# Kernel optimization log

Measured on AMD Instinct MI355X. Metric: run time of the kernel, lower is better.

Reference implementation:

```python
import jax, jax.numpy as jnp
import numpy as np

NUM_GROUPS = 32
EPS = 1e-6


def group_norm(x, gamma, beta):
    # x: [b, c, d, h, w]
    b, c, d, h, w = x.shape
    xg = x.reshape(b, NUM_GROUPS, c // NUM_GROUPS, d, h, w)
    mean = jnp.mean(xg, axis=(2, 3, 4, 5), keepdims=True)
    var = jnp.var(xg, axis=(2, 3, 4, 5), keepdims=True)
    xn = ((xg - mean) * jax.lax.rsqrt(var + EPS)).reshape(b, c, d, h, w)
    return xn * gamma[None, :, None, None, None] + beta[None, :, None, None, None]


def conv1x1(x, w, bias):
    # 1x1x1 conv == channel-mixing matmul. x: [b,c,d,h,w], w: [co,ci]
    y = jnp.einsum('oc,bcdhw->bodhw', w, x)
    return y + bias[None, :, None, None, None]


def setup_inputs() -> dict:
    key = jax.random.key(0)
    ks = jax.random.split(key, 12)
    b, c, d, h, w = 2, 512, 16, 16, 16
    scale = 1.0 / np.sqrt(c)
    inp = {
        'x': jax.random.normal(ks[0], (b, c, d, h, w), dtype=jnp.float32),
        'gamma': jnp.ones((c,), dtype=jnp.float32),
        'beta': jnp.zeros((c,), dtype=jnp.float32),
        'wq': jax.random.normal(ks[1], (c, c), dtype=jnp.float32) * scale,
        'bq': jnp.zeros((c,), dtype=jnp.float32),
        'wk': jax.random.normal(ks[2], (c, c), dtype=jnp.float32) * scale,
        'bk': jnp.zeros((c,), dtype=jnp.float32),
        'wv': jax.random.normal(ks[3], (c, c), dtype=jnp.float32) * scale,
        'bv': jnp.zeros((c,), dtype=jnp.float32),
        'wo': jax.random.normal(ks[4], (c, c), dtype=jnp.float32) * scale,
        'bo': jnp.zeros((c,), dtype=jnp.float32),
    }
    return inp


def reference(x, gamma, beta, wq, bq, wk, bk, wv, bv, wo, bo):
    b, c, d, h, w = x.shape
    n = d * h * w
    h_ = group_norm(x, gamma, beta)
    q = conv1x1(h_, wq, bq).reshape(b, c, n)  # [b,c,n]
    k = conv1x1(h_, wk, bk).reshape(b, c, n)
    v = conv1x1(h_, wv, bv).reshape(b, c, n)
    scale = jnp.float32(c) ** -0.5
    # attn[b, i, j] = sum_c q[b,c,i] * k[b,c,j]
    attn = jnp.einsum('bci,bcj->bij', q, k) * scale
    attn = jax.nn.softmax(attn, axis=2)
    # out[b, c, i] = sum_j attn[b,i,j] * v[b,c,j]
    o = jnp.einsum('bij,bcj->bci', attn, v).reshape(b, c, d, h, w)
    return x + conv1x1(o, wo, bo)
```

## Files before the change

kernel.cpp:

```cpp
#include <hip/hip_runtime.h>
#include <hip/hip_bf16.h>

typedef __bf16 bf16x8 __attribute__((ext_vector_type(8)));
typedef _Float16 f16x8 __attribute__((ext_vector_type(8)));
typedef unsigned short u16x8 __attribute__((ext_vector_type(8)));
typedef float f32x4 __attribute__((ext_vector_type(4)));
using bf16 = __hip_bfloat16;

constexpr int Cdim = 512;
constexpr int Nsp  = 4096;
constexpr int NB   = 2;
constexpr float SCALE = 0.04419417382415922f;
constexpr int EPITCH = 132;

#define GL2LDS(gaddr, laddr)                                                              \
    __builtin_amdgcn_global_load_lds((const __attribute__((address_space(1))) void*)(gaddr), \
                                     (__attribute__((address_space(3))) void*)(laddr), 16, 0, 0)

#define STG1(dst, src, ld) { int _o = tid * 16, _r = _o >> 7, _c = ((_o >> 4) ^ _r) & 7;      \
    GL2LDS((const unsigned short*)(src) + (size_t)_r * (ld) + _c * 8,                          \
           (unsigned short*)(dst) + (_o >> 1)); }

__global__ __launch_bounds__(256) void k_cvt_all(const float* __restrict__ wq, const float* __restrict__ wk,
                                                 const float* __restrict__ wv, const float* __restrict__ wo,
                                                 bf16* __restrict__ wqkb, bf16* __restrict__ wvb,
                                                 bf16* __restrict__ wob, float* __restrict__ lsum) {
    if (blockIdx.x >= 256) {
        #pragma unroll
        for (int j = 0; j < 8; ++j)
            ((float4*)lsum)[8 * threadIdx.x + j] = float4{0.f, 0.f, 0.f, 0.f};
        return;
    }
    int i = blockIdx.x * 256 + threadIdx.x;
    float4 q = ((const float4*)wq)[i];
    float4 k = ((const float4*)wk)[i];
    float4 v = ((const float4*)wv)[i];
    float4 o = ((const float4*)wo)[i];
    bf16* dq = wqkb + (size_t)i * 4;
    dq[0] = __float2bfloat16(q.x); dq[1] = __float2bfloat16(q.y);
    dq[2] = __float2bfloat16(q.z); dq[3] = __float2bfloat16(q.w);
    bf16* dk = wqkb + 262144 + (size_t)i * 4;
    dk[0] = __float2bfloat16(k.x); dk[1] = __float2bfloat16(k.y);
    dk[2] = __float2bfloat16(k.z); dk[3] = __float2bfloat16(k.w);
    bf16* dv = wvb + (size_t)i * 4;
    dv[0] = __float2bfloat16(v.x); dv[1] = __float2bfloat16(v.y);
    dv[2] = __float2bfloat16(v.z); dv[3] = __float2bfloat16(v.w);
    bf16* dw = wob + (size_t)i * 4;
    dw[0] = __float2bfloat16(o.x); dw[1] = __float2bfloat16(o.y);
    dw[2] = __float2bfloat16(o.z); dw[3] = __float2bfloat16(o.w);
}

__global__ __launch_bounds__(256) void k_gn_stats(const float* __restrict__ x, float* __restrict__ stats) {
    int bg = blockIdx.x;
    const float4* p = (const float4*)(x + (size_t)bg * (16 * 4096));
    float s = 0.f, s2 = 0.f;
    for (int i = threadIdx.x; i < 16384; i += 256) {
        float4 v = p[i];
        s  += v.x + v.y + v.z + v.w;
        s2 += v.x * v.x + v.y * v.y + v.z * v.z + v.w * v.w;
    }
    #pragma unroll
    for (int off = 32; off; off >>= 1) { s += __shfl_xor(s, off); s2 += __shfl_xor(s2, off); }
    __shared__ float rs[4], rs2[4];
    int w = threadIdx.x >> 6;
    if ((threadIdx.x & 63) == 0) { rs[w] = s; rs2[w] = s2; }
    __syncthreads();
    if (threadIdx.x == 0) {
        float S = rs[0] + rs[1] + rs[2] + rs[3];
        float S2 = rs2[0] + rs2[1] + rs2[2] + rs2[3];
        float mean = S * (1.f / 65536.f);
        float var  = S2 * (1.f / 65536.f) - mean * mean;
        stats[bg * 2]     = mean;
        stats[bg * 2 + 1] = rsqrtf(var + 1e-6f);
    }
}

__global__ __launch_bounds__(256) void k_gn_apply(const float* __restrict__ x, const float* __restrict__ stats,
                                                  const float* __restrict__ gamma, const float* __restrict__ beta,
                                                  bf16* __restrict__ ht) {
    int b = blockIdx.y;
    int n0 = blockIdx.x * 64;
    int tid = threadIdx.x;
    __shared__ float tile[64][65];
    int nn_l = tid & 63, cc0 = tid >> 6;
    int cc_w = tid & 63, nn0 = tid >> 6;
    for (int c0 = 0; c0 < Cdim; c0 += 64) {
        #pragma unroll
        for (int p = 0; p < 16; ++p) {
            int cc = p * 4 + cc0;
            tile[cc][nn_l] = x[(size_t)(b * Cdim + c0 + cc) * Nsp + n0 + nn_l];
        }
        __syncthreads();
        int c = c0 + cc_w, g = c >> 4;
        float mean = stats[(b * 32 + g) * 2];
        float rstd = stats[(b * 32 + g) * 2 + 1];
        float ga = gamma[c], be = beta[c];
        #pragma unroll
        for (int p = 0; p < 16; ++p) {
            int nn = p * 4 + nn0;
            float v = tile[cc_w][nn];
            ht[(size_t)(b * Nsp + n0 + nn) * Cdim + c] = __float2bfloat16((v - mean) * rstd * ga + be);
        }
        __syncthreads();
    }
}

template <int DT>
__device__ __forceinline__ f32x4 mma16(u16x8 a, u16x8 b, f32x4 c) {
    if constexpr (DT == 0)
        return __builtin_amdgcn_mfma_f32_16x16x32_bf16(__builtin_bit_cast(bf16x8, a),
                                                       __builtin_bit_cast(bf16x8, b), c, 0, 0, 0);
    else
        return __builtin_amdgcn_mfma_f32_16x16x32_f16(__builtin_bit_cast(f16x8, a),
                                                      __builtin_bit_cast(f16x8, b), c, 0, 0, 0);
}

template <int BM, int DT, int OUTT, int BIAS, int RESID, int SPLITK, int EXPSUM>
__global__ __launch_bounds__(256) void k_gemm_nt(
    const void* __restrict__ Av, long long As, int lda,
    const void* __restrict__ Bv, long long Bs, int ldb,
    const float* __restrict__ bias, const float* __restrict__ bias2,
    const float* __restrict__ resid, long long Rs,
    float* __restrict__ lsum,
    void* __restrict__ outv, long long Os,
    int N, int K) {
    constexpr int MT = BM / 32;
    constexpr int SME_STAGE = (BM + 128) * 64;
    constexpr int SME_EPI   = BM * EPITCH;
    constexpr int SME = SME_STAGE > SME_EPI ? SME_STAGE : SME_EPI;
    const int bm = blockIdx.x, bn = blockIdx.y, zz = blockIdx.z;
    const int bt  = (SPLITK > 1) ? (zz % NB) : zz;
    const int ksl = (SPLITK > 1) ? (zz / NB) : 0;
    const int Kc = K / SPLITK;
    const int kbeg = ksl * Kc;
    const unsigned short* Ab = (const unsigned short*)Av + (size_t)bt * As;
    const unsigned short* Bb = (const unsigned short*)Bv + (size_t)bt * Bs;
    const int tid = threadIdx.x, lane = tid & 63, w = tid >> 6;
    const int quad = lane >> 4, l16 = lane & 15;
    const int wm = w >> 1, wn = w & 1;
    __shared__ __align__(16) unsigned short smem[SME];
    unsigned short (*Asub)[64] = (unsigned short(*)[64])smem;
    unsigned short (*Bsub)[64] = (unsigned short(*)[64])(smem + BM * 64);
    f32x4 zero4 = {0.f, 0.f, 0.f, 0.f};
    f32x4 acc[MT][4];
    #pragma unroll
    for (int i = 0; i < MT; ++i)
        #pragma unroll
        for (int j = 0; j < 4; ++j) acc[i][j] = zero4;
    const int row0 = bm * BM, col0 = bn * 128;
    const size_t ldab = (size_t)lda * 2, ldbb = (size_t)ldb * 2;
    const int lsw = (l16 & 7) * 8;
    for (int k0 = kbeg; k0 < kbeg + Kc; k0 += 64) {
        const char* Abase = (const char*)Ab + (size_t)k0 * 2;
        const char* Bbase = (const char*)Bb + (size_t)k0 * 2;
        #pragma unroll
        for (int p = 0; p < BM / 32; ++p) {
            int o = p * 4096 + tid * 16;
            int r = o >> 7;
            int cs = ((o >> 4) ^ r) & 7;
            GL2LDS(Abase + (size_t)(row0 + r) * ldab + cs * 16, (char*)smem + o);
        }
        #pragma unroll
        for (int p = 0; p < 4; ++p) {
            int o = p * 4096 + tid * 16;
            int r = o >> 7;
            int cs = ((o >> 4) ^ r) & 7;
            GL2LDS(Bbase + (size_t)(col0 + r) * ldbb + cs * 16, (char*)smem + BM * 128 + o);
        }
        __syncthreads();
        #pragma unroll
        for (int ks = 0; ks < 2; ++ks) {
            u16x8 af[MT], bfr[4];
            #pragma unroll
            for (int t = 0; t < MT; ++t)
                af[t] = *(const u16x8*)&Asub[wm * (BM / 2) + t * 16 + l16][(ks * 32 + quad * 8) ^ lsw];
            #pragma unroll
            for (int t = 0; t < 4; ++t)
                bfr[t] = *(const u16x8*)&Bsub[wn * 64 + t * 16 + l16][(ks * 32 + quad * 8) ^ lsw];
            #pragma unroll
            for (int tm = 0; tm < MT; ++tm)
                #pragma unroll
                for (int tn = 0; tn < 4; ++tn) acc[tm][tn] = mma16<DT>(af[tm], bfr[tn], acc[tm][tn]);
        }
        __syncthreads();
    }

    if constexpr (OUTT == 2) {
        #pragma unroll
        for (int tm = 0; tm < MT; ++tm)
            #pragma unroll
            for (int tn = 0; tn < 4; ++tn)
                #pragma unroll
                for (int r = 0; r < 4; ++r) {
                    int row = row0 + wm * (BM / 2) + tm * 16 + quad * 4 + r;
                    int col = col0 + wn * 64 + tn * 16 + l16;
                    float v = acc[tm][tn][r];
                    if constexpr (BIAS == 1) v += bias[row];
                    else if constexpr (BIAS == 2) v += bias[col];
                    if constexpr (RESID) v += resid[(size_t)bt * Rs + (size_t)row * N + col];
                    ((float*)outv)[(size_t)zz * Os + (size_t)row * N + col] = v;
                }
    } else {
        #pragma unroll
        for (int tn = 0; tn < 4; ++tn) {
            int colL = wn * 64 + tn * 16 + l16;
            float bc = 0.f;
            if constexpr (BIAS == 2) bc = bias[col0 + colL];
            else if constexpr (BIAS == 3) {
                int col = col0 + colL;
                bc = (col < 512) ? bias[col] : bias2[col - 512];
            }
            #pragma unroll
            for (int tm = 0; tm < MT; ++tm)
                #pragma unroll
                for (int r = 0; r < 4; ++r) {
                    int rowL = wm * (BM / 2) + tm * 16 + quad * 4 + r;
                    float v = acc[tm][tn][r];
                    if constexpr (BIAS == 1) v += bias[row0 + rowL];
                    else if constexpr (BIAS == 2) v += bc;
                    else if constexpr (BIAS == 3) {
                        int col = col0 + colL;
                        v = (col < 512) ? (v + bc) * SCALE : v + bc;
                    }
                    if constexpr (EXPSUM) v = __expf(v);
                    unsigned short hv;
                    if constexpr (OUTT == 1) { _Float16 h = (_Float16)v; hv = __builtin_bit_cast(unsigned short, h); }
                    else { bf16 h = __float2bfloat16(v); hv = __builtin_bit_cast(unsigned short, h); }
                    smem[rowL * EPITCH + colL] = hv;
                }
        }
        __syncthreads();
        const int cch = (tid & 15) * 8;
        const int rg  = (tid >> 4) * (BM / 16);
        #pragma unroll
        for (int i = 0; i < BM / 16; ++i) {
            int rowL = rg + i;
            u16x8 hv = *(const u16x8*)&smem[rowL * EPITCH + cch];
            *(u16x8*)((unsigned short*)outv + (size_t)zz * Os + (size_t)(row0 + rowL) * N + col0 + cch) = hv;
            if constexpr (EXPSUM) {
                float ps = 0.f;
                #pragma unroll
                for (int e = 0; e < 8; ++e) {
                    bf16 h = __builtin_bit_cast(bf16, hv[e]);
                    ps += __bfloat162float(h);
                }
                #pragma unroll
                for (int m = 1; m < 16; m <<= 1) ps += __shfl_xor(ps, m);
                if ((lane & 15) == 0) atomicAdd(lsum + (size_t)bt * Nsp + row0 + rowL, ps);
            }
        }
    }
}

__global__ __launch_bounds__(512, 2) void k_attn(const bf16* __restrict__ QKt_, const bf16* __restrict__ Vm_,
                                                 float* __restrict__ lsum, bf16* __restrict__ Opart_) {
    constexpr int NT = 32;
    const int bx = blockIdx.x, js = blockIdx.y, bt = blockIdx.z;
    const int i0 = bx * 64;
    const int jbase = js * 2048;
    const unsigned short* Qb = (const unsigned short*)QKt_ + (size_t)bt * ((size_t)Nsp * 1024);
    const unsigned short* Vb = (const unsigned short*)Vm_ + (size_t)bt * ((size_t)Nsp * Cdim);
    const int tid = threadIdx.x, lane = tid & 63, w = tid >> 6;
    const int quad = lane >> 4, l16 = lane & 15;
    const int wm = w >> 2, wn = w & 3;
    const int lsw = (l16 & 7) * 8;
    __shared__ __align__(16) unsigned short smem[69632];
    unsigned short* Q_l = smem;
    unsigned short* H0  = smem + 32768;
    unsigned short* H1  = smem + 49152;
    unsigned short* P_l = smem + 65536;

#define FR(sub, row, kc) (*(const u16x8*)&(sub)[(row) * 64 + ((kc) ^ lsw)])
#define PH_TOP() \
    __builtin_amdgcn_s_barrier(); \
    asm volatile("s_waitcnt lgkmcnt(0)" ::: "memory"); \
    __builtin_amdgcn_sched_barrier(0); \
    __builtin_amdgcn_s_setprio(1);

    f32x4 zero4 = {0.f, 0.f, 0.f, 0.f};
    f32x4 acc[2][8];
    #pragma unroll
    for (int m = 0; m < 2; ++m)
        #pragma unroll
        for (int n = 0; n < 8; ++n) acc[m][n] = zero4;
    float rsum[2][4] = {{0.f, 0.f, 0.f, 0.f}, {0.f, 0.f, 0.f, 0.f}};
    u16x8 pa[2][2];
    u16x8 fb[8];

    #pragma unroll
    for (int s = 0; s < 8; ++s) STG1(Q_l + s * 4096, Qb + (size_t)i0 * 1024 + s * 64, 1024);
    #pragma unroll
    for (int s = 0; s < 4; ++s) STG1(H0 + s * 4096, Qb + (size_t)jbase * 1024 + 512 + s * 64, 1024);
    asm volatile("s_waitcnt vmcnt(0)" ::: "memory");
    __builtin_amdgcn_s_barrier();
    __builtin_amdgcn_sched_barrier(0);

    for (int t = 0; t < NT; ++t) {
        const int j0 = jbase + t * 64;
        f32x4 aS[2] = {zero4, zero4};
        #pragma unroll
        for (int ks = 0; ks < 8; ++ks)
            fb[ks] = FR(H0 + (ks >> 1) * 4096, wn * 16 + l16, (ks & 1) * 32 + quad * 8);
        #pragma unroll
        for (int s = 0; s < 4; ++s)
            STG1(H1 + s * 4096, Qb + (size_t)j0 * 1024 + 512 + 256 + s * 64, 1024);
        PH_TOP();
        #pragma unroll
        for (int ks = 0; ks < 8; ++ks)
            #pragma unroll
            for (int m = 0; m < 2; ++m) {
                u16x8 aq = FR(Q_l + (ks >> 1) * 4096, wm * 32 + m * 16 + l16, (ks & 1) * 32 + quad * 8);
                aS[m] = mma16<0>(aq, fb[ks], aS[m]);
            }
        __builtin_amdgcn_s_setprio(0);
        asm volatile("s_waitcnt vmcnt(0)" ::: "memory");
        __builtin_amdgcn_s_barrier();
        #pragma unroll
        for (int ks = 0; ks < 8; ++ks)
            fb[ks] = FR(H1 + (ks >> 1) * 4096, wn * 16 + l16, (ks & 1) * 32 + quad * 8);
        #pragma unroll
        for (int s = 0; s < 4; ++s)
            STG1(H0 + s * 4096, Vb + (size_t)(s * 64) * 4096 + j0, 4096);
        PH_TOP();
        #pragma unroll
        for (int ks = 0; ks < 8; ++ks)
            #pragma unroll
            for (int m = 0; m < 2; ++m) {
                u16x8 aq = FR(Q_l + (4 + (ks >> 1)) * 4096, wm * 32 + m * 16 + l16, (ks & 1) * 32 + quad * 8);
                aS[m] = mma16<0>(aq, fb[ks], aS[m]);
            }
        __builtin_amdgcn_s_setprio(0);
        __builtin_amdgcn_s_barrier();
        #pragma unroll
        for (int s = 0; s < 4; ++s)
            STG1(H1 + s * 4096, Vb + (size_t)(256 + s * 64) * 4096 + j0, 4096);
        #pragma unroll
        for (int m = 0; m < 2; ++m)
            #pragma unroll
            for (int r = 0; r < 4; ++r) {
                float p = __expf(aS[m][r]);
                rsum[m][r] += p;
                int il = wm * 32 + m * 16 + quad * 4 + r;
                bf16 h = __float2bfloat16(p);
                P_l[il * 64 + ((wn * 16 + l16) ^ ((il & 7) * 8))] = __builtin_bit_cast(unsigned short, h);
            }
        asm volatile("s_waitcnt lgkmcnt(0)" ::: "memory");
        asm volatile("s_waitcnt vmcnt(4)" ::: "memory");
        __builtin_amdgcn_s_barrier();
        __builtin_amdgcn_sched_barrier(0);
        #pragma unroll
        for (int nn = 0; nn < 4; ++nn)
            #pragma unroll
            for (int ks = 0; ks < 2; ++ks)
                fb[nn * 2 + ks] = FR(H0 + wn * 4096, nn * 16 + l16, ks * 32 + quad * 8);
        PH_TOP();
        #pragma unroll
        for (int m = 0; m < 2; ++m)
            #pragma unroll
            for (int ks = 0; ks < 2; ++ks)
                pa[m][ks] = *(const u16x8*)&P_l[(wm * 32 + m * 16 + l16) * 64 + ((ks * 32 + quad * 8) ^ lsw)];
        #pragma unroll
        for (int m = 0; m < 2; ++m)
            #pragma unroll
            for (int nn = 0; nn < 4; ++nn)
                #pragma unroll
                for (int ks = 0; ks < 2; ++ks)
                    acc[m][nn] = mma16<0>(pa[m][ks], fb[nn * 2 + ks], acc[m][nn]);
        __builtin_amdgcn_s_setprio(0);
        asm volatile("s_waitcnt vmcnt(0)" ::: "memory");
        __builtin_amdgcn_s_barrier();
        #pragma unroll
        for (int nn = 0; nn < 4; ++nn)
            #pragma unroll
            for (int ks = 0; ks < 2; ++ks)
                fb[nn * 2 + ks] = FR(H1 + wn * 4096, nn * 16 + l16, ks * 32 + quad * 8);
        if (t + 1 < NT) {
            #pragma unroll
            for (int s = 0; s < 4; ++s)
                STG1(H0 + s * 4096, Qb + (size_t)(j0 + 64) * 1024 + 512 + s * 64, 1024);
        }
        PH_TOP();
        #pragma unroll
        for (int m = 0; m < 2; ++m)
            #pragma unroll
            for (int nn = 0; nn < 4; ++nn)
                #pragma unroll
                for (int ks = 0; ks < 2; ++ks)
                    acc[m][4 + nn] = mma16<0>(pa[m][ks], fb[nn * 2 + ks], acc[m][4 + nn]);
        __builtin_amdgcn_s_setprio(0);
        asm volatile("s_waitcnt vmcnt(0)" ::: "memory");
        __builtin_amdgcn_s_barrier();
        __builtin_amdgcn_sched_barrier(0);
    }
#undef FR
#undef PH_TOP

    #pragma unroll
    for (int m = 0; m < 2; ++m)
        #pragma unroll
        for (int r = 0; r < 4; ++r) {
            float v = rsum[m][r];
            v += __shfl_xor(v, 1); v += __shfl_xor(v, 2); v += __shfl_xor(v, 4); v += __shfl_xor(v, 8);
            if (l16 == 0)
                atomicAdd(lsum + (size_t)bt * Nsp + i0 + wm * 32 + m * 16 + quad * 4 + r, v);
        }
    __syncthreads();
    #pragma unroll
    for (int m = 0; m < 2; ++m)
        #pragma unroll
        for (int h = 0; h < 2; ++h)
            #pragma unroll
            for (int nn = 0; nn < 4; ++nn) {
                int colL = h * 256 + wn * 64 + nn * 16 + l16;
                int rowB = wm * 32 + m * 16 + quad * 4;
                #pragma unroll
                for (int r = 0; r < 4; ++r) {
                    int rw = rowB + r;
                    bf16 hv = __float2bfloat16(acc[m][h * 4 + nn][r]);
                    smem[rw * 520 + (colL ^ ((rw & 7) * 8))] = __builtin_bit_cast(unsigned short, hv);
                }
            }
    __syncthreads();
    const int orow = tid >> 3, ocb = tid & 7;
    unsigned short* od = (unsigned short*)Opart_ + (size_t)js * ((size_t)NB * Nsp * Cdim) +
                         ((size_t)bt * Nsp + i0 + orow) * Cdim;
    #pragma unroll
    for (int it = 0; it < 8; ++it) {
        int cc = ocb + it * 8;
        u16x8 hv = *(const u16x8*)&smem[orow * 520 + ((cc * 8) ^ ((orow & 7) * 8))];
        *(u16x8*)(od + cc * 8) = hv;
    }
}

__global__ __launch_bounds__(256) void k_reduce2(const bf16* __restrict__ P, const float* __restrict__ lsum,
                                                 bf16* __restrict__ O) {
    constexpr size_t SL = (size_t)NB * Nsp * Cdim;
    size_t i = ((size_t)blockIdx.x * 256 + threadIdx.x) * 8;
    float linv = 1.f / lsum[i >> 9];
    union { bf16 h[8]; uint4 u; } a, b, r;
    a.u = *(const uint4*)(P + i);
    b.u = *(const uint4*)(P + SL + i);
    #pragma unroll
    for (int e = 0; e < 8; ++e) {
        float s = __bfloat162float(a.h[e]) + __bfloat162float(b.h[e]);
        r.h[e] = __float2bfloat16(s * linv);
    }
    *(uint4*)(O + i) = r.u;
}

extern "C" void kernel_launch(void* const* d_in, const int* in_sizes, int n_in,
                              void* d_out, int out_size, void* d_ws, size_t ws_size,
                              hipStream_t stream) {
    const float* x     = (const float*)d_in[0];
    const float* gamma = (const float*)d_in[1];
    const float* beta  = (const float*)d_in[2];
    const float* wq = (const float*)d_in[3];  const float* bq = (const float*)d_in[4];
    const float* wk = (const float*)d_in[5];  const float* bk = (const float*)d_in[6];
    const float* wv = (const float*)d_in[7];  const float* bv = (const float*)d_in[8];
    const float* wo = (const float*)d_in[9];  const float* bo = (const float*)d_in[10];
    float* out = (float*)d_out;

    char* ws = (char*)d_ws;
    float* stats = (float*)ws;
    size_t off = 1024;
    float* lsum = (float*)(ws + off); off += (size_t)NB * Nsp * 4 + 1024;
    bf16* wqkb = (bf16*)(ws + off); off += (size_t)1024 * 512 * 2;
    bf16* wvb  = (bf16*)(ws + off); off += (size_t)512 * 512 * 2;
    bf16* wob  = (bf16*)(ws + off); off += (size_t)512 * 512 * 2;
    bf16* Vm   = (bf16*)(ws + off); off += (size_t)NB * Nsp * Cdim * 2;
    bf16* Ot   = (bf16*)(ws + off); off += (size_t)NB * Nsp * Cdim * 2;
    bf16* Opart = (bf16*)(ws + off); off += (size_t)2 * NB * Nsp * Cdim * 2;
    bf16* ht   = (bf16*)(ws + off); off += (size_t)NB * Nsp * Cdim * 2;
    bf16* QKt  = (bf16*)(ws + off); off += (size_t)NB * Nsp * 1024 * 2;

    k_cvt_all<<<257, 256, 0, stream>>>(wq, wk, wv, wo, wqkb, wvb, wob, lsum);
    k_gn_stats<<<64, 256, 0, stream>>>(x, stats);
    k_gn_apply<<<dim3(64, 2), 256, 0, stream>>>(x, stats, gamma, beta, ht);

    const long long hs = (long long)Nsp * Cdim;
    const long long qs = (long long)Nsp * 1024;

    k_gemm_nt<128, 0, 0, 3, 0, 1, 0><<<dim3(32, 8, 2), 256, 0, stream>>>(
        ht, hs, 512, wqkb, 0, 512, bq, bk, nullptr, 0, nullptr, QKt, qs, 1024, 512);
    k_gemm_nt<128, 0, 0, 1, 0, 1, 0><<<dim3(4, 32, 2), 256, 0, stream>>>(
        wvb, 0, 512, ht, hs, 512, bv, nullptr, nullptr, 0, nullptr, Vm, hs, 4096, 512);
    k_attn<<<dim3(64, 2, 2), 512, 0, stream>>>(QKt, Vm, lsum, Opart);
    k_reduce2<<<2048, 256, 0, stream>>>(Opart, lsum, Ot);
    k_gemm_nt<128, 0, 2, 1, 1, 1, 0><<<dim3(4, 32, 2), 256, 0, stream>>>(
        wob, 0, 512, Ot, hs, 512, bo, nullptr, x, hs, nullptr, out, hs, 4096, 512);
}
```

Before: 253.1 us.

## Hold Q fragments in registers and deepen K/V prefetch across four LDS slots

The attention kernel now loads its Q tile from LDS into registers once (qa[2][16]), which frees the Q region of shared memory. That space is reused so K halves and V halves each get their own buffer, four slots in total. Global-to-LDS loads for the next K/V pieces are issued earlier and tracked with partial vmcnt waits instead of full drains, aiming to overlap memory traffic with MFMA work and remove stalls. The cost is many more VGPRs for the Q fragments, which may cut occupancy or cause spills at launch_bounds(512,2), and more fragile wait-count bookkeeping.

```diff
diff --git a/kernel.cpp b/kernel.cpp
--- a/kernel.cpp
+++ b/kernel.cpp
@@ -265,17 +265,20 @@
     const int wm = w >> 2, wn = w & 3;
     const int lsw = (l16 & 7) * 8;
     __shared__ __align__(16) unsigned short smem[69632];
-    unsigned short* Q_l = smem;
-    unsigned short* H0  = smem + 32768;
-    unsigned short* H1  = smem + 49152;
     unsigned short* P_l = smem + 65536;
 
-#define FR(sub, row, kc) (*(const u16x8*)&(sub)[(row) * 64 + ((kc) ^ lsw)])
-#define PH_TOP() \
-    __builtin_amdgcn_s_barrier(); \
-    asm volatile("s_waitcnt lgkmcnt(0)" ::: "memory"); \
-    __builtin_amdgcn_sched_barrier(0); \
-    __builtin_amdgcn_s_setprio(1);
+    auto stgK = [&](int jj, int dh, unsigned short* dst) {
+        #pragma unroll
+        for (int s = 0; s < 4; ++s)
+            STG1(dst + s * 4096, Qb + (size_t)jj * 1024 + 512 + dh * 256 + s * 64, 1024);
+    };
+    auto stgV = [&](int jj, int ch, unsigned short* dst) {
+        #pragma unroll
+        for (int s = 0; s < 4; ++s)
+            STG1(dst + s * 4096, Vb + (size_t)(ch * 256 + s * 64) * 4096 + jj, 4096);
+    };
+
+#define FRD(base, row, kc) (*(const u16x8*)&(base)[(row) * 64 + ((kc) ^ lsw)])
 
     f32x4 zero4 = {0.f, 0.f, 0.f, 0.f};
     f32x4 acc[2][8];
@@ -285,55 +288,74 @@
         for (int n = 0; n < 8; ++n) acc[m][n] = zero4;
     float rsum[2][4] = {{0.f, 0.f, 0.f, 0.f}, {0.f, 0.f, 0.f, 0.f}};
     u16x8 pa[2][2];
-    u16x8 fb[8];
-
-    #pragma unroll
-    for (int s = 0; s < 8; ++s) STG1(Q_l + s * 4096, Qb + (size_t)i0 * 1024 + s * 64, 1024);
-    #pragma unroll
-    for (int s = 0; s < 4; ++s) STG1(H0 + s * 4096, Qb + (size_t)jbase * 1024 + 512 + s * 64, 1024);
-    asm volatile("s_waitcnt vmcnt(0)" ::: "memory");
+
+    #pragma unroll
+    for (int s = 0; s < 8; ++s) STG1(smem + s * 4096, Qb + (size_t)i0 * 1024 + s * 64, 1024);
+    stgK(jbase, 0, smem + 2 * 16384);
+    stgK(jbase, 1, smem + 3 * 16384);
+    asm volatile("s_waitcnt vmcnt(8)" ::: "memory");
     __builtin_amdgcn_s_barrier();
     __builtin_amdgcn_sched_barrier(0);
+    u16x8 qa[2][16];
+    #pragma unroll
+    for (int m = 0; m < 2; ++m)
+        #pragma unroll
+        for (int ks = 0; ks < 16; ++ks)
+            qa[m][ks] = FRD(smem + (ks >> 1) * 4096, wm * 32 + m * 16 + l16, (ks & 1) * 32 + quad * 8);
+    asm volatile("s_waitcnt lgkmcnt(0)" ::: "memory");
+    __builtin_amdgcn_s_barrier();
+    __builtin_amdgcn_sched_barrier(0);
+    stgV(jbase, 0, smem);
+
+#define PH_WAIT(N) \
+    asm volatile("s_waitcnt vmcnt(" #N ")" ::: "memory"); \
+    __builtin_amdgcn_s_barrier(); \
+    __builtin_amdgcn_sched_barrier(0);
+#define S_CLUSTER(KSL, QOFF) { \
+    u16x8 kb[8]; \
+    _Pragma("unroll") \
+    for (int ks = 0; ks < 8; ++ks) \
+        kb[ks] = FRD((KSL) + (ks >> 1) * 4096, wn * 16 + l16, (ks & 1) * 32 + quad * 8); \
+    asm volatile("s_waitcnt lgkmcnt(0)" ::: "memory"); \
+    __builtin_amdgcn_sched_barrier(0); \
+    __builtin_amdgcn_s_setprio(1); \
+    _Pragma("unroll") \
+    for (int ks = 0; ks < 8; ++ks) \
+        _Pragma("unroll") \
+        for (int m = 0; m < 2; ++m) aS[m] = mma16<0>(qa[m][(QOFF) + ks], kb[ks], aS[m]); \
+    __builtin_amdgcn_s_setprio(0); \
+    __builtin_amdgcn_s_barrier(); }
+#define PV_CLUSTER(VSL, HOFF) { \
+    u16x8 fb[4][2]; \
+    _Pragma("unroll") \
+    for (int nn = 0; nn < 4; ++nn) \
+        _Pragma("unroll") \
+        for (int ks = 0; ks < 2; ++ks) \
+            fb[nn][ks] = FRD((VSL) + wn * 4096, nn * 16 + l16, ks * 32 + quad * 8); \
+    asm volatile("s_waitcnt lgkmcnt(0)" ::: "memory"); \
+    __builtin_amdgcn_sched_barrier(0); \
+    __builtin_amdgcn_s_setprio(1); \
+    _Pragma("unroll") \
+    for (int m = 0; m < 2; ++m) \
+        _Pragma("unroll") \
+        for (int nn = 0; nn < 4; ++nn) \
+            _Pragma("unroll") \
+            for (int ks = 0; ks < 2; ++ks) \
+                acc[m][(HOFF) + nn] = mma16<0>(pa[m][ks], fb[nn][ks], acc[m][(HOFF) + nn]); \
+    __builtin_amdgcn_s_setprio(0); \
+    __builtin_amdgcn_s_barrier(); }
 
     for (int t = 0; t < NT; ++t) {
         const int j0 = jbase + t * 64;
+        const int j1 = j0 + 64;
         f32x4 aS[2] = {zero4, zero4};
-        #pragma unroll
-        for (int ks = 0; ks < 8; ++ks)
-            fb[ks] = FR(H0 + (ks >> 1) * 4096, wn * 16 + l16, (ks & 1) * 32 + quad * 8);
-        #pragma unroll
-        for (int s = 0; s < 4; ++s)
-            STG1(H1 + s * 4096, Qb + (size_t)j0 * 1024 + 512 + 256 + s * 64, 1024);
-        PH_TOP();
-        #pragma unroll
-        for (int ks = 0; ks < 8; ++ks)
-            #pragma unroll
-            for (int m = 0; m < 2; ++m) {
-                u16x8 aq = FR(Q_l + (ks >> 1) * 4096, wm * 32 + m * 16 + l16, (ks & 1) * 32 + quad * 8);
-                aS[m] = mma16<0>(aq, fb[ks], aS[m]);
-            }
-        __builtin_amdgcn_s_setprio(0);
-        asm volatile("s_waitcnt vmcnt(0)" ::: "memory");
-        __builtin_amdgcn_s_barrier();
-        #pragma unroll
-        for (int ks = 0; ks < 8; ++ks)
-            fb[ks] = FR(H1 + (ks >> 1) * 4096, wn * 16 + l16, (ks & 1) * 32 + quad * 8);
-        #pragma unroll
-        for (int s = 0; s < 4; ++s)
-            STG1(H0 + s * 4096, Vb + (size_t)(s * 64) * 4096 + j0, 4096);
-        PH_TOP();
-        #pragma unroll
-        for (int ks = 0; ks < 8; ++ks)
-            #pragma unroll
-            for (int m = 0; m < 2; ++m) {
-                u16x8 aq = FR(Q_l + (4 + (ks >> 1)) * 4096, wm * 32 + m * 16 + l16, (ks & 1) * 32 + quad * 8);
-                aS[m] = mma16<0>(aq, fb[ks], aS[m]);
-            }
-        __builtin_amdgcn_s_setprio(0);
-        __builtin_amdgcn_s_barrier();
-        #pragma unroll
-        for (int s = 0; s < 4; ++s)
-            STG1(H1 + s * 4096, Vb + (size_t)(256 + s * 64) * 4096 + j0, 4096);
+        stgV(j0, 1, smem + 1 * 16384);
+        PH_WAIT(12)
+        S_CLUSTER(smem + 2 * 16384, 0)
+        if (t + 1 < NT) { stgK(j1, 0, smem + 2 * 16384); PH_WAIT(12) }
+        else            { PH_WAIT(8) }
+        S_CLUSTER(smem + 3 * 16384, 8)
+        if (t + 1 < NT) stgK(j1, 1, smem + 3 * 16384);
         #pragma unroll
         for (int m = 0; m < 2; ++m)
             #pragma unroll
@@ -345,55 +367,21 @@
                 P_l[il * 64 + ((wn * 16 + l16) ^ ((il & 7) * 8))] = __builtin_bit_cast(unsigned short, h);
             }
         asm volatile("s_waitcnt lgkmcnt(0)" ::: "memory");
-        asm volatile("s_waitcnt vmcnt(4)" ::: "memory");
-        __builtin_amdgcn_s_barrier();
-        __builtin_amdgcn_sched_barrier(0);
-        #pragma unroll
-        for (int nn = 0; nn < 4; ++nn)
-            #pragma unroll
-            for (int ks = 0; ks < 2; ++ks)
-                fb[nn * 2 + ks] = FR(H0 + wn * 4096, nn * 16 + l16, ks * 32 + quad * 8);
-        PH_TOP();
+        if (t + 1 < NT) { PH_WAIT(12) } else { PH_WAIT(4) }
         #pragma unroll
         for (int m = 0; m < 2; ++m)
             #pragma unroll
             for (int ks = 0; ks < 2; ++ks)
                 pa[m][ks] = *(const u16x8*)&P_l[(wm * 32 + m * 16 + l16) * 64 + ((ks * 32 + quad * 8) ^ lsw)];
-        #pragma unroll
-        for (int m = 0; m < 2; ++m)
-            #pragma unroll
-            for (int nn = 0; nn < 4; ++nn)
-                #pragma unroll
-                for (int ks = 0; ks < 2; ++ks)
-                    acc[m][nn] = mma16<0>(pa[m][ks], fb[nn * 2 + ks], acc[m][nn]);
-        __builtin_amdgcn_s_setprio(0);
-        asm volatile("s_waitcnt vmcnt(0)" ::: "memory");
-        __builtin_amdgcn_s_barrier();
-        #pragma unroll
-        for (int nn = 0; nn < 4; ++nn)
-            #pragma unroll
-            for (int ks = 0; ks < 2; ++ks)
-                fb[nn * 2 + ks] = FR(H1 + wn * 4096, nn * 16 + l16, ks * 32 + quad * 8);
-        if (t + 1 < NT) {
-            #pragma unroll
-            for (int s = 0; s < 4; ++s)
-                STG1(H0 + s * 4096, Qb + (size_t)(j0 + 64) * 1024 + 512 + s * 64, 1024);
-        }
-        PH_TOP();
-        #pragma unroll
-        for (int m = 0; m < 2; ++m)
-            #pragma unroll
-            for (int nn = 0; nn < 4; ++nn)
-                #pragma unroll
-                for (int ks = 0; ks < 2; ++ks)
-                    acc[m][4 + nn] = mma16<0>(pa[m][ks], fb[nn * 2 + ks], acc[m][4 + nn]);
-        __builtin_amdgcn_s_setprio(0);
-        asm volatile("s_waitcnt vmcnt(0)" ::: "memory");
-        __builtin_amdgcn_s_barrier();
-        __builtin_amdgcn_sched_barrier(0);
-    }
-#undef FR
-#undef PH_TOP
+        PV_CLUSTER(smem, 0)
+        if (t + 1 < NT) { stgV(j1, 0, smem); PH_WAIT(12) }
+        else            { PH_WAIT(0) }
+        PV_CLUSTER(smem + 1 * 16384, 4)
+    }
+#undef FRD
+#undef PH_WAIT
+#undef S_CLUSTER
+#undef PV_CLUSTER
 
     #pragma unroll
     for (int m = 0; m < 2; ++m)
```

Result: slower. 345.4 us (+36.5%).

## Triple-buffer K/V tiles with rotating LDS buffers and register-resident Q fragment

Applied to the files above, without the earlier changes.

Restructures the attention main loop into a three-buffer rotation (A/B/C) so each K or V half-tile load is issued two phases ahead, with partial vmcnt waits instead of full drains. The low half of Q is held in registers for the whole loop, freeing the LDS space that backs the third buffer, while the high half of Q stays in LDS. This aims to hide global-to-LDS latency and cut stalls at barriers. In exchange it raises register pressure from the extra Q fragments, which at launch bounds of 512 threads and 2 blocks could cause spills, and the vmcnt accounting is fragile.

```diff
diff --git a/kernel.cpp b/kernel.cpp
--- a/kernel.cpp
+++ b/kernel.cpp
@@ -265,17 +265,25 @@
     const int wm = w >> 2, wn = w & 3;
     const int lsw = (l16 & 7) * 8;
     __shared__ __align__(16) unsigned short smem[69632];
-    unsigned short* Q_l = smem;
-    unsigned short* H0  = smem + 32768;
-    unsigned short* H1  = smem + 49152;
+    unsigned short* Qhi = smem + 49152;
     unsigned short* P_l = smem + 65536;
 
-#define FR(sub, row, kc) (*(const u16x8*)&(sub)[(row) * 64 + ((kc) ^ lsw)])
-#define PH_TOP() \
+    auto stgK = [&](int jj, int dh, unsigned short* dst) {
+        #pragma unroll
+        for (int s = 0; s < 4; ++s)
+            STG1(dst + s * 4096, Qb + (size_t)jj * 1024 + 512 + dh * 256 + s * 64, 1024);
+    };
+    auto stgV = [&](int jj, int ch, unsigned short* dst) {
+        #pragma unroll
+        for (int s = 0; s < 4; ++s)
+            STG1(dst + s * 4096, Vb + (size_t)(ch * 256 + s * 64) * 4096 + jj, 4096);
+    };
+
+#define FRD(base, row, kc) (*(const u16x8*)&(base)[(row) * 64 + ((kc) ^ lsw)])
+#define WAIT_BAR(N) \
+    asm volatile("s_waitcnt vmcnt(" #N ")" ::: "memory"); \
     __builtin_amdgcn_s_barrier(); \
-    asm volatile("s_waitcnt lgkmcnt(0)" ::: "memory"); \
-    __builtin_amdgcn_sched_barrier(0); \
-    __builtin_amdgcn_s_setprio(1);
+    __builtin_amdgcn_sched_barrier(0);
 
     f32x4 zero4 = {0.f, 0.f, 0.f, 0.f};
     f32x4 acc[2][8];
@@ -285,55 +293,69 @@
         for (int n = 0; n < 8; ++n) acc[m][n] = zero4;
     float rsum[2][4] = {{0.f, 0.f, 0.f, 0.f}, {0.f, 0.f, 0.f, 0.f}};
     u16x8 pa[2][2];
-    u16x8 fb[8];
-
-    #pragma unroll
-    for (int s = 0; s < 8; ++s) STG1(Q_l + s * 4096, Qb + (size_t)i0 * 1024 + s * 64, 1024);
-    #pragma unroll
-    for (int s = 0; s < 4; ++s) STG1(H0 + s * 4096, Qb + (size_t)jbase * 1024 + 512 + s * 64, 1024);
-    asm volatile("s_waitcnt vmcnt(0)" ::: "memory");
+
+    unsigned short* A = smem;
+    unsigned short* B = smem + 16384;
+    unsigned short* C = smem + 32768;
+
+    #pragma unroll
+    for (int s = 0; s < 4; ++s) STG1(C + s * 4096, Qb + (size_t)i0 * 1024 + s * 64, 1024);
+    #pragma unroll
+    for (int s = 0; s < 4; ++s) STG1(Qhi + s * 4096, Qb + (size_t)i0 * 1024 + 256 + s * 64, 1024);
+    stgK(jbase, 0, A);
+    stgK(jbase, 1, B);
+    WAIT_BAR(8)
+    u16x8 qa[2][8];
+    #pragma unroll
+    for (int m = 0; m < 2; ++m)
+        #pragma unroll
+        for (int ks = 0; ks < 8; ++ks)
+            qa[m][ks] = FRD(C + (ks >> 1) * 4096, wm * 32 + m * 16 + l16, (ks & 1) * 32 + quad * 8);
+    asm volatile("s_waitcnt lgkmcnt(0)" ::: "memory");
     __builtin_amdgcn_s_barrier();
     __builtin_amdgcn_sched_barrier(0);
 
     for (int t = 0; t < NT; ++t) {
         const int j0 = jbase + t * 64;
+        const int j1 = j0 + 64;
         f32x4 aS[2] = {zero4, zero4};
-        #pragma unroll
-        for (int ks = 0; ks < 8; ++ks)
-            fb[ks] = FR(H0 + (ks >> 1) * 4096, wn * 16 + l16, (ks & 1) * 32 + quad * 8);
-        #pragma unroll
-        for (int s = 0; s < 4; ++s)
-            STG1(H1 + s * 4096, Qb + (size_t)j0 * 1024 + 512 + 256 + s * 64, 1024);
-        PH_TOP();
-        #pragma unroll
-        for (int ks = 0; ks < 8; ++ks)
-            #pragma unroll
-            for (int m = 0; m < 2; ++m) {
-                u16x8 aq = FR(Q_l + (ks >> 1) * 4096, wm * 32 + m * 16 + l16, (ks & 1) * 32 + quad * 8);
-                aS[m] = mma16<0>(aq, fb[ks], aS[m]);
-            }
-        __builtin_amdgcn_s_setprio(0);
-        asm volatile("s_waitcnt vmcnt(0)" ::: "memory");
-        __builtin_amdgcn_s_barrier();
-        #pragma unroll
-        for (int ks = 0; ks < 8; ++ks)
-            fb[ks] = FR(H1 + (ks >> 1) * 4096, wn * 16 + l16, (ks & 1) * 32 + quad * 8);
-        #pragma unroll
-        for (int s = 0; s < 4; ++s)
-            STG1(H0 + s * 4096, Vb + (size_t)(s * 64) * 4096 + j0, 4096);
-        PH_TOP();
-        #pragma unroll
-        for (int ks = 0; ks < 8; ++ks)
-            #pragma unroll
-            for (int m = 0; m < 2; ++m) {
-                u16x8 aq = FR(Q_l + (4 + (ks >> 1)) * 4096, wm * 32 + m * 16 + l16, (ks & 1) * 32 + quad * 8);
-                aS[m] = mma16<0>(aq, fb[ks], aS[m]);
-            }
-        __builtin_amdgcn_s_setprio(0);
-        __builtin_amdgcn_s_barrier();
-        #pragma unroll
-        for (int s = 0; s < 4; ++s)
-            STG1(H1 + s * 4096, Vb + (size_t)(256 + s * 64) * 4096 + j0, 4096);
+        WAIT_BAR(4)
+        stgV(j0, 0, C);
+        {
+            u16x8 kb[8];
+            #pragma unroll
+            for (int ks = 0; ks < 8; ++ks)
+                kb[ks] = FRD(A + (ks >> 1) * 4096, wn * 16 + l16, (ks & 1) * 32 + quad * 8);
+            asm volatile("s_waitcnt lgkmcnt(0)" ::: "memory");
+            __builtin_amdgcn_sched_barrier(0);
+            __builtin_amdgcn_s_setprio(1);
+            #pragma unroll
+            for (int ks = 0; ks < 8; ++ks)
+                #pragma unroll
+                for (int m = 0; m < 2; ++m) aS[m] = mma16<0>(qa[m][ks], kb[ks], aS[m]);
+            __builtin_amdgcn_s_setprio(0);
+        }
+        WAIT_BAR(4)
+        stgV(j0, 1, A);
+        {
+            u16x8 kb[8];
+            #pragma unroll
+            for (int ks = 0; ks < 8; ++ks)
+                kb[ks] = FRD(B + (ks >> 1) * 4096, wn * 16 + l16, (ks & 1) * 32 + quad * 8);
+            asm volatile("s_waitcnt lgkmcnt(0)" ::: "memory");
+            __builtin_amdgcn_sched_barrier(0);
+            __builtin_amdgcn_s_setprio(1);
+            #pragma unroll
+            for (int ks = 0; ks < 8; ++ks)
+                #pragma unroll
+                for (int m = 0; m < 2; ++m) {
+                    u16x8 aq = FRD(Qhi + (ks >> 1) * 4096, wm * 32 + m * 16 + l16, (ks & 1) * 32 + quad * 8);
+                    aS[m] = mma16<0>(aq, kb[ks], aS[m]);
+                }
+            __builtin_amdgcn_s_setprio(0);
+        }
+        WAIT_BAR(4)
+        if (t + 1 < NT) stgK(j1, 0, B);
         #pragma unroll
         for (int m = 0; m < 2; ++m)
             #pragma unroll
@@ -345,55 +367,57 @@
                 P_l[il * 64 + ((wn * 16 + l16) ^ ((il & 7) * 8))] = __builtin_bit_cast(unsigned short, h);
             }
         asm volatile("s_waitcnt lgkmcnt(0)" ::: "memory");
-        asm volatile("s_waitcnt vmcnt(4)" ::: "memory");
         __builtin_amdgcn_s_barrier();
         __builtin_amdgcn_sched_barrier(0);
-        #pragma unroll
-        for (int nn = 0; nn < 4; ++nn)
-            #pragma unroll
-            for (int ks = 0; ks < 2; ++ks)
-                fb[nn * 2 + ks] = FR(H0 + wn * 4096, nn * 16 + l16, ks * 32 + quad * 8);
-        PH_TOP();
-        #pragma unroll
-        for (int m = 0; m < 2; ++m)
-            #pragma unroll
-            for (int ks = 0; ks < 2; ++ks)
-                pa[m][ks] = *(const u16x8*)&P_l[(wm * 32 + m * 16 + l16) * 64 + ((ks * 32 + quad * 8) ^ lsw)];
-        #pragma unroll
-        for (int m = 0; m < 2; ++m)
+        {
+            u16x8 fb[4][2];
             #pragma unroll
             for (int nn = 0; nn < 4; ++nn)
                 #pragma unroll
                 for (int ks = 0; ks < 2; ++ks)
-                    acc[m][nn] = mma16<0>(pa[m][ks], fb[nn * 2 + ks], acc[m][nn]);
-        __builtin_amdgcn_s_setprio(0);
-        asm volatile("s_waitcnt vmcnt(0)" ::: "memory");
-        __builtin_amdgcn_s_barrier();
-        #pragma unroll
-        for (int nn = 0; nn < 4; ++nn)
-            #pragma unroll
-            for (int ks = 0; ks < 2; ++ks)
-                fb[nn * 2 + ks] = FR(H1 + wn * 4096, nn * 16 + l16, ks * 32 + quad * 8);
-        if (t + 1 < NT) {
-            #pragma unroll
-            for (int s = 0; s < 4; ++s)
-                STG1(H0 + s * 4096, Qb + (size_t)(j0 + 64) * 1024 + 512 + s * 64, 1024);
-        }
-        PH_TOP();
-        #pragma unroll
-        for (int m = 0; m < 2; ++m)
+                    fb[nn][ks] = FRD(C + wn * 4096, nn * 16 + l16, ks * 32 + quad * 8);
+            #pragma unroll
+            for (int m = 0; m < 2; ++m)
+                #pragma unroll
+                for (int ks = 0; ks < 2; ++ks)
+                    pa[m][ks] = *(const u16x8*)&P_l[(wm * 32 + m * 16 + l16) * 64 + ((ks * 32 + quad * 8) ^ lsw)];
+            asm volatile("s_waitcnt lgkmcnt(0)" ::: "memory");
+            __builtin_amdgcn_sched_barrier(0);
+            __builtin_amdgcn_s_setprio(1);
+            #pragma unroll
+            for (int m = 0; m < 2; ++m)
+                #pragma unroll
+                for (int nn = 0; nn < 4; ++nn)
+                    #pragma unroll
+                    for (int ks = 0; ks < 2; ++ks)
+                        acc[m][nn] = mma16<0>(pa[m][ks], fb[nn][ks], acc[m][nn]);
+            __builtin_amdgcn_s_setprio(0);
+        }
+        if (t + 1 < NT) { WAIT_BAR(4) } else { WAIT_BAR(0) }
+        if (t + 1 < NT) stgK(j1, 1, C);
+        {
+            u16x8 fb[4][2];
             #pragma unroll
             for (int nn = 0; nn < 4; ++nn)
                 #pragma unroll
                 for (int ks = 0; ks < 2; ++ks)
-                    acc[m][4 + nn] = mma16<0>(pa[m][ks], fb[nn * 2 + ks], acc[m][4 + nn]);
-        __builtin_amdgcn_s_setprio(0);
-        asm volatile("s_waitcnt vmcnt(0)" ::: "memory");
-        __builtin_amdgcn_s_barrier();
-        __builtin_amdgcn_sched_barrier(0);
-    }
-#undef FR
-#undef PH_TOP
+                    fb[nn][ks] = FRD(A + wn * 4096, nn * 16 + l16, ks * 32 + quad * 8);
+            asm volatile("s_waitcnt lgkmcnt(0)" ::: "memory");
+            __builtin_amdgcn_sched_barrier(0);
+            __builtin_amdgcn_s_setprio(1);
+            #pragma unroll
+            for (int m = 0; m < 2; ++m)
+                #pragma unroll
+                for (int nn = 0; nn < 4; ++nn)
+                    #pragma unroll
+                    for (int ks = 0; ks < 2; ++ks)
+                        acc[m][4 + nn] = mma16<0>(pa[m][ks], fb[nn][ks], acc[m][4 + nn]);
+            __builtin_amdgcn_s_setprio(0);
+        }
+        unsigned short* tmp = A; A = B; B = C; C = tmp;
+    }
+#undef FRD
+#undef WAIT_BAR
 
     #pragma unroll
     for (int m = 0; m < 2; ++m)
```

Result: no change. 249.1 us (-1.6%).
